# Performance work log

Hardware: AMD Instinct MI355X
Metric: run time of the kernel (lower is better)

## Reference

```python
import jax, jax.numpy as jnp
import numpy as np
import math

B, S, D = 4, 2048, 1024


def setup_inputs() -> dict:
    key = jax.random.key(0)
    k1, k2, k3 = jax.random.split(key, 3)
    X = jax.random.normal(k1, (B, S, D), dtype=jnp.float32)
    # causal mask, broadcast over batch (True = keep)
    mask = jnp.broadcast_to(jnp.tril(jnp.ones((S, S), dtype=bool)), (B, S, S))
    # torch nn.Linear weights: y = x @ W.T; init scale ~ 1/sqrt(D)
    WQK = jax.random.normal(k2, (D, D), dtype=jnp.float32) / math.sqrt(D)
    WOV = jax.random.normal(k3, (D, D), dtype=jnp.float32) / math.sqrt(D)
    return {"X": X, "mask": mask, "WQK": WQK, "WOV": WOV}


def reference(X, mask, WQK, WOV):
    d = X.shape[-1]
    Q = jnp.einsum('bsd,ed->bse', X, WQK)          # WQK(X) = X @ WQK.T
    Sc = jnp.einsum('bse,bte->bst', Q, X)          # shared-QK scores: Q @ X^T
    # NOTE: original multiplies by sqrt(d_model) (not divide) - faithful
    Sc = Sc * jnp.asarray(math.sqrt(d), Sc.dtype)
    Sc = jnp.where(mask, Sc, -jnp.inf)
    A = jax.nn.softmax(Sc, axis=-1)                # dropout p=0.0 -> identity
    V = jnp.einsum('bsd,ed->bse', X, WOV)          # WOV(X)
    Y = jnp.einsum('bst,bte->bse', A, V)
    return (X + Y, A)
```

## Files before the change

kernel.cpp:

```cpp
#include <hip/hip_runtime.h>
#include <hip/hip_fp16.h>
#include <math.h>

typedef _Float16 half_t;
typedef _Float16 h8_t __attribute__((ext_vector_type(8)));
typedef _Float16 h4_t __attribute__((ext_vector_type(4)));
typedef float f4_t __attribute__((ext_vector_type(4)));

#define MFMA16(a, b, c) __builtin_amdgcn_mfma_f32_16x16x32_f16(a, b, c, 0, 0, 0)

static constexpr int kB = 4;
static constexpr int kS = 2048;
static constexpr int kD = 1024;
static constexpr int BM = 128;
static constexpr int BN = 128;
static constexpr int BK = 32;
static constexpr int NT = 512;

__device__ __forceinline__ void gload16(const half_t* g, half_t* l) {
  __builtin_amdgcn_global_load_lds(
      (const __attribute__((address_space(1))) void*)g,
      (__attribute__((address_space(3))) void*)l, 16, 0, 0);
}

__device__ __forceinline__ void stage_tile(half_t* __restrict__ sm,
                                           const half_t* __restrict__ g, int ld) {
  const int t = threadIdx.x;
  const int r = t >> 2;
  const int c = ((t & 3) * 8) ^ ((((r >> 1) & 3)) << 3);
  gload16(&g[(size_t)r * ld + c], &sm[r * BK + (t & 3) * 8]);
}

template <bool SPLIT>
__device__ __forceinline__ void stage_all(half_t* buf, const half_t* Ahi,
                                          const half_t* Alo, int lda,
                                          const half_t* Bhi, const half_t* Blo,
                                          int ldb, size_t ko) {
  stage_tile(buf, Ahi + ko, lda);
  stage_tile(buf + BM * BK, Bhi + ko, ldb);
  if (SPLIT) {
    stage_tile(buf + 2 * BM * BK, Alo + ko, lda);
    stage_tile(buf + 3 * BM * BK, Blo + ko, ldb);
  }
}

template <bool SPLIT>
__device__ __forceinline__ void gemm_core(const half_t* __restrict__ Ahi,
                                          const half_t* __restrict__ Alo, int lda,
                                          const half_t* __restrict__ Bhi,
                                          const half_t* __restrict__ Blo, int ldb,
                                          int k_iters, half_t* sm, f4_t acc[4][2]) {
  constexpr int BUFSZ = (SPLIT ? 4 : 2) * BM * BK;
  const int lane = threadIdx.x & 63;
  const int wid = threadIdx.x >> 6;
  const int wm = (wid >> 2) * 64;
  const int wn = (wid & 3) * 32;
  const int fr = lane & 15;
  const int fk = (((lane >> 4) * 8) ^ (((lane >> 1) & 3) << 3));

  half_t* cur = sm;
  half_t* nxt = sm + BUFSZ;

  stage_all<SPLIT>(cur, Ahi, Alo, lda, Bhi, Blo, ldb, 0);
  asm volatile("s_waitcnt vmcnt(0)" ::: "memory");
  __builtin_amdgcn_s_barrier();

  for (int kk = 0; kk < k_iters; ++kk) {
    if (kk + 1 < k_iters)
      stage_all<SPLIT>(nxt, Ahi, Alo, lda, Bhi, Blo, ldb, (size_t)(kk + 1) * BK);
    const half_t* sAh = cur;
    const half_t* sBh = cur + BM * BK;
    const half_t* sAl = cur + 2 * BM * BK;
    const half_t* sBl = cur + 3 * BM * BK;
    h8_t a[4], b[2], al[4], bl[2];
#pragma unroll
    for (int i = 0; i < 4; ++i) {
      a[i] = *(const h8_t*)&sAh[(wm + i * 16 + fr) * BK + fk];
      if (SPLIT) al[i] = *(const h8_t*)&sAl[(wm + i * 16 + fr) * BK + fk];
    }
#pragma unroll
    for (int j = 0; j < 2; ++j) {
      b[j] = *(const h8_t*)&sBh[(wn + j * 16 + fr) * BK + fk];
      if (SPLIT) bl[j] = *(const h8_t*)&sBl[(wn + j * 16 + fr) * BK + fk];
    }
#pragma unroll
    for (int i = 0; i < 4; ++i)
#pragma unroll
      for (int j = 0; j < 2; ++j) {
        acc[i][j] = MFMA16(a[i], b[j], acc[i][j]);
        if (SPLIT) {
          acc[i][j] = MFMA16(a[i], bl[j], acc[i][j]);
          acc[i][j] = MFMA16(al[i], b[j], acc[i][j]);
        }
      }
    asm volatile("s_waitcnt vmcnt(0)" ::: "memory");
    __builtin_amdgcn_s_barrier();
    half_t* t = cur; cur = nxt; nxt = t;
  }
}

__global__ __launch_bounds__(NT) void gemm_q_kernel(
    const half_t* __restrict__ Xhi, const half_t* __restrict__ Xlo,
    const half_t* __restrict__ Whi, const half_t* __restrict__ Wlo,
    half_t* __restrict__ Qhi, half_t* __restrict__ Qlo) {
  __shared__ half_t sm[2 * 4 * BM * BK];
  const size_t arow = (size_t)blockIdx.y * BM;
  const size_t brow = (size_t)blockIdx.x * BN;
  f4_t acc[4][2] = {};
  gemm_core<true>(Xhi + arow * kD, Xlo + arow * kD, kD,
                  Whi + brow * kD, Wlo + brow * kD, kD, kD / BK, sm, acc);
  const int lane = threadIdx.x & 63;
  const int wid = threadIdx.x >> 6;
  const int wm = (wid >> 2) * 64, wn = (wid & 3) * 32;
  const int c16 = lane & 15, r4 = (lane >> 4) * 4;
#pragma unroll
  for (int i = 0; i < 4; ++i)
#pragma unroll
    for (int j = 0; j < 2; ++j)
#pragma unroll
      for (int r = 0; r < 4; ++r) {
        const size_t row = arow + wm + i * 16 + r4 + r;
        const size_t col = brow + wn + j * 16 + c16;
        const float q = acc[i][j][r];
        const half_t qh = (half_t)q;
        const half_t ql = (half_t)(q - (float)qh);
        const size_t idx = row * kD + col;
        Qhi[idx] = qh;
        Qlo[idx] = ql;
      }
}

__global__ __launch_bounds__(NT) void gemm_v_kernel(
    const half_t* __restrict__ Xhi, const half_t* __restrict__ Whi,
    half_t* __restrict__ Vt) {
  __shared__ half_t sm[2 * 2 * BM * BK];
  const size_t arow = (size_t)blockIdx.y * BM;
  const size_t brow = (size_t)blockIdx.x * BN;
  f4_t acc[4][2] = {};
  gemm_core<false>(Xhi + arow * kD, nullptr, kD, Whi + brow * kD, nullptr, kD,
                   kD / BK, sm, acc);
  const int lane = threadIdx.x & 63;
  const int wid = threadIdx.x >> 6;
  const int wm = (wid >> 2) * 64, wn = (wid & 3) * 32;
  const int c16 = lane & 15, r4 = (lane >> 4) * 4;
#pragma unroll
  for (int i = 0; i < 4; ++i)
#pragma unroll
    for (int j = 0; j < 2; ++j)
#pragma unroll
      for (int r = 0; r < 4; ++r) {
        const size_t row = arow + wm + i * 16 + r4 + r;
        const size_t col = brow + wn + j * 16 + c16;
        const size_t bi = row >> 11;
        const size_t s = row & 2047;
        Vt[bi * (size_t)kD * kS + col * kS + s] = (half_t)acc[i][j][r];
      }
}

__global__ __launch_bounds__(NT) void gemm_score_kernel(
    const half_t* __restrict__ Qhi, const half_t* __restrict__ Qlo,
    const half_t* __restrict__ Xhi, const half_t* __restrict__ Xlo,
    float* __restrict__ Sc) {
  const int tn = blockIdx.x, tm = blockIdx.y, bi = blockIdx.z;
  if (tn > tm) return;
  __shared__ half_t sm[2 * 4 * BM * BK];
  const size_t arow = (size_t)bi * kS + (size_t)tm * BM;
  const size_t brow = (size_t)bi * kS + (size_t)tn * BN;
  f4_t acc[4][2] = {};
  gemm_core<true>(Qhi + arow * kD, Qlo + arow * kD, kD,
                  Xhi + brow * kD, Xlo + brow * kD, kD, kD / BK, sm, acc);
  float* out = Sc + (size_t)bi * kS * kS;
  const int lane = threadIdx.x & 63;
  const int wid = threadIdx.x >> 6;
  const int wm = (wid >> 2) * 64, wn = (wid & 3) * 32;
  const int c16 = lane & 15, r4 = (lane >> 4) * 4;
#pragma unroll
  for (int i = 0; i < 4; ++i)
#pragma unroll
    for (int j = 0; j < 2; ++j)
#pragma unroll
      for (int r = 0; r < 4; ++r) {
        const int row = tm * BM + wm + i * 16 + r4 + r;
        const int col = tn * BN + wn + j * 16 + c16;
        out[(size_t)row * kS + col] = 32.0f * acc[i][j][r];
      }
}

__global__ __launch_bounds__(256) void softmax_kernel(float* __restrict__ A,
                                                      half_t* __restrict__ Ah) {
  const int rgl = blockIdx.x;
  const int s = rgl & 2047;
  float* row = A + (size_t)rgl * kS;
  half_t* hrow = Ah + (size_t)rgl * kS;
  const int tid = threadIdx.x;
  const int n = s + 1;
  float v[8];
  float mx = -INFINITY;
#pragma unroll
  for (int i = 0; i < 8; ++i) {
    const int t = tid + i * 256;
    v[i] = (t < n) ? row[t] : -INFINITY;
    mx = fmaxf(mx, v[i]);
  }
  for (int off = 32; off; off >>= 1) mx = fmaxf(mx, __shfl_xor(mx, off));
  __shared__ float red[8];
  const int lane = tid & 63, wid = tid >> 6;
  if (lane == 0) red[wid] = mx;
  __syncthreads();
  if (tid == 0) {
    float m = fmaxf(fmaxf(red[0], red[1]), fmaxf(red[2], red[3]));
    red[4] = m;
  }
  __syncthreads();
  mx = red[4];
  float sum = 0.0f;
#pragma unroll
  for (int i = 0; i < 8; ++i) {
    v[i] = (tid + i * 256 < n) ? __expf(v[i] - mx) : 0.0f;
    sum += v[i];
  }
  for (int off = 32; off; off >>= 1) sum += __shfl_xor(sum, off);
  __syncthreads();
  if (lane == 0) red[wid] = sum;
  __syncthreads();
  if (tid == 0) red[5] = 1.0f / (red[0] + red[1] + red[2] + red[3]);
  __syncthreads();
  const float inv = red[5];
#pragma unroll
  for (int i = 0; i < 8; ++i) {
    const int t = tid + i * 256;
    const float a = v[i] * inv;
    row[t] = a;
    hrow[t] = (half_t)a;
  }
}

__global__ __launch_bounds__(NT) void gemm_y_kernel(
    const half_t* __restrict__ Ah, const half_t* __restrict__ Vt,
    const float* __restrict__ X, float* __restrict__ Out) {
  __shared__ half_t sm[2 * 2 * BM * BK];
  const int tn = blockIdx.x, bi = blockIdx.z;
  const int tm = (kS / BM - 1) - blockIdx.y;
  const size_t abase = ((size_t)bi * kS + (size_t)tm * BM) * kS;
  const size_t bbase = ((size_t)bi * kD + (size_t)tn * BN) * kS;
  f4_t acc[4][2] = {};
  gemm_core<false>(Ah + abase, nullptr, kS, Vt + bbase, nullptr, kS,
                   (tm + 1) * BM / BK, sm, acc);
  const size_t obase = (size_t)bi * kS * kD;
  const int lane = threadIdx.x & 63;
  const int wid = threadIdx.x >> 6;
  const int wm = (wid >> 2) * 64, wn = (wid & 3) * 32;
  const int c16 = lane & 15, r4 = (lane >> 4) * 4;
#pragma unroll
  for (int i = 0; i < 4; ++i)
#pragma unroll
    for (int j = 0; j < 2; ++j)
#pragma unroll
      for (int r = 0; r < 4; ++r) {
        const size_t row = (size_t)tm * BM + wm + i * 16 + r4 + r;
        const size_t col = (size_t)tn * BN + wn + j * 16 + c16;
        const size_t idx = obase + row * kD + col;
        Out[idx] = X[idx] + acc[i][j][r];
      }
}

__global__ __launch_bounds__(256) void split_kernel(const float* __restrict__ x,
                                                    half_t* __restrict__ hi,
                                                    half_t* __restrict__ lo, int n4) {
  const int i = blockIdx.x * 256 + threadIdx.x;
  if (i >= n4) return;
  const float4 v = ((const float4*)x)[i];
  const float vv[4] = {v.x, v.y, v.z, v.w};
  h4_t h, l;
#pragma unroll
  for (int j = 0; j < 4; ++j) {
    const half_t hh = (half_t)vv[j];
    h[j] = hh;
    l[j] = (half_t)(vv[j] - (float)hh);
  }
  ((h4_t*)hi)[i] = h;
  ((h4_t*)lo)[i] = l;
}

__global__ __launch_bounds__(256) void cvt_kernel(const float* __restrict__ x,
                                                  half_t* __restrict__ hi, int n4) {
  const int i = blockIdx.x * 256 + threadIdx.x;
  if (i >= n4) return;
  const float4 v = ((const float4*)x)[i];
  h4_t h;
  h[0] = (half_t)v.x; h[1] = (half_t)v.y; h[2] = (half_t)v.z; h[3] = (half_t)v.w;
  ((h4_t*)hi)[i] = h;
}

extern "C" void kernel_launch(void* const* d_in, const int* in_sizes, int n_in,
                              void* d_out, int out_size, void* d_ws, size_t ws_size,
                              hipStream_t stream) {
  const float* X   = (const float*)d_in[0];
  const float* WQK = (const float*)d_in[2];
  const float* WOV = (const float*)d_in[3];

  constexpr size_t nX = (size_t)kB * kS * kD;
  constexpr size_t nW = (size_t)kD * kD;
  constexpr size_t nA = (size_t)kB * kS * kS;

  float* out0 = (float*)d_out;
  float* outA = out0 + nX;

  half_t* ws = (half_t*)d_ws;
  half_t* Xhi = ws; ws += nX;
  half_t* Xlo = ws; ws += nX;
  half_t* Qhi = ws; ws += nX;
  half_t* Qlo = ws; ws += nX;
  half_t* Whi = ws; ws += nW;
  half_t* Wlo = ws; ws += nW;
  half_t* WVh = ws; ws += nW;
  half_t* Vt  = ws; ws += nX;
  half_t* Ah  = ws; ws += nA;
  const size_t need_bytes = (size_t)((char*)ws - (char*)d_ws);
  if (ws_size < need_bytes) return;

  split_kernel<<<(int)(nX / 4 / 256), 256, 0, stream>>>(X, Xhi, Xlo, (int)(nX / 4));
  split_kernel<<<(int)(nW / 4 / 256), 256, 0, stream>>>(WQK, Whi, Wlo, (int)(nW / 4));
  cvt_kernel<<<(int)(nW / 4 / 256), 256, 0, stream>>>(WOV, WVh, (int)(nW / 4));

  gemm_q_kernel<<<dim3(kD / BN, kB * kS / BM), NT, 0, stream>>>(Xhi, Xlo, Whi, Wlo, Qhi, Qlo);
  gemm_v_kernel<<<dim3(kD / BN, kB * kS / BM), NT, 0, stream>>>(Xhi, WVh, Vt);
  gemm_score_kernel<<<dim3(kS / BN, kS / BM, kB), NT, 0, stream>>>(Qhi, Qlo, Xhi, Xlo, outA);
  softmax_kernel<<<kB * kS, 256, 0, stream>>>(outA, Ah);
  gemm_y_kernel<<<dim3(kD / BN, kS / BM, kB), NT, 0, stream>>>(Ah, Vt, X, out0);
}
```

Measured before the change: 380.0 us.

## Use 64x64 tiles for split-precision GEMMs, vectorize softmax, fuse prep kernels

The Q and score GEMMs, which use three-MFMA hi/lo split precision, move from 128x128 tiles with 512 threads to 64x64 tiles with 256 threads and a min-blocks launch bound, so more blocks run and the causal triangle is covered at finer granularity. The softmax now loads and stores contiguous 8-element chunks with vector accesses instead of strided scalar ones. The three input-conversion kernels are merged into one launch. Smaller tiles cut data reuse per block and raise global and LDS traffic per FLOP.

```diff
diff --git a/kernel.cpp b/kernel.cpp
--- a/kernel.cpp
+++ b/kernel.cpp
@@ -12,10 +12,7 @@
 static constexpr int kB = 4;
 static constexpr int kS = 2048;
 static constexpr int kD = 1024;
-static constexpr int BM = 128;
-static constexpr int BN = 128;
 static constexpr int BK = 32;
-static constexpr int NT = 512;
 
 __device__ __forceinline__ void gload16(const half_t* g, half_t* l) {
   __builtin_amdgcn_global_load_lds(
@@ -23,75 +20,68 @@
       (__attribute__((address_space(3))) void*)l, 16, 0, 0);
 }
 
-__device__ __forceinline__ void stage_tile(half_t* __restrict__ sm,
-                                           const half_t* __restrict__ g, int ld) {
+
+__device__ __forceinline__ void stage_tile64(half_t* __restrict__ sm,
+                                             const half_t* __restrict__ g, int ld) {
   const int t = threadIdx.x;
   const int r = t >> 2;
-  const int c = ((t & 3) * 8) ^ ((((r >> 1) & 3)) << 3);
-  gload16(&g[(size_t)r * ld + c], &sm[r * BK + (t & 3) * 8]);
-}
-
-template <bool SPLIT>
-__device__ __forceinline__ void stage_all(half_t* buf, const half_t* Ahi,
+  const int g8 = (t & 3) * 8;
+  const int c = g8 ^ (((r >> 1) & 3) << 3);
+  gload16(&g[(size_t)r * ld + c], &sm[r * BK + g8]);
+}
+
+__device__ __forceinline__ void stage4_64(half_t* buf, const half_t* Ahi,
                                           const half_t* Alo, int lda,
                                           const half_t* Bhi, const half_t* Blo,
                                           int ldb, size_t ko) {
-  stage_tile(buf, Ahi + ko, lda);
-  stage_tile(buf + BM * BK, Bhi + ko, ldb);
-  if (SPLIT) {
-    stage_tile(buf + 2 * BM * BK, Alo + ko, lda);
-    stage_tile(buf + 3 * BM * BK, Blo + ko, ldb);
-  }
-}
-
-template <bool SPLIT>
-__device__ __forceinline__ void gemm_core(const half_t* __restrict__ Ahi,
-                                          const half_t* __restrict__ Alo, int lda,
-                                          const half_t* __restrict__ Bhi,
-                                          const half_t* __restrict__ Blo, int ldb,
-                                          int k_iters, half_t* sm, f4_t acc[4][2]) {
-  constexpr int BUFSZ = (SPLIT ? 4 : 2) * BM * BK;
-  const int lane = threadIdx.x & 63;
-  const int wid = threadIdx.x >> 6;
-  const int wm = (wid >> 2) * 64;
-  const int wn = (wid & 3) * 32;
+  stage_tile64(buf,               Ahi + ko, lda);
+  stage_tile64(buf + 64 * BK,     Bhi + ko, ldb);
+  stage_tile64(buf + 2 * 64 * BK, Alo + ko, lda);
+  stage_tile64(buf + 3 * 64 * BK, Blo + ko, ldb);
+}
+
+__device__ __forceinline__ void gemm64_core(const half_t* __restrict__ Ahi,
+                                            const half_t* __restrict__ Alo, int lda,
+                                            const half_t* __restrict__ Bhi,
+                                            const half_t* __restrict__ Blo, int ldb,
+                                            int k_iters, half_t* sm, f4_t (&acc)[2][2]) {
+  constexpr int BUFSZ = 4 * 64 * BK;
+  const int lane = threadIdx.x & 63;
+  const int wid = threadIdx.x >> 6;
+  const int wm = (wid >> 1) * 32;
+  const int wn = (wid & 1) * 32;
   const int fr = lane & 15;
   const int fk = (((lane >> 4) * 8) ^ (((lane >> 1) & 3) << 3));
 
   half_t* cur = sm;
   half_t* nxt = sm + BUFSZ;
 
-  stage_all<SPLIT>(cur, Ahi, Alo, lda, Bhi, Blo, ldb, 0);
+  stage4_64(cur, Ahi, Alo, lda, Bhi, Blo, ldb, 0);
   asm volatile("s_waitcnt vmcnt(0)" ::: "memory");
   __builtin_amdgcn_s_barrier();
 
   for (int kk = 0; kk < k_iters; ++kk) {
     if (kk + 1 < k_iters)
-      stage_all<SPLIT>(nxt, Ahi, Alo, lda, Bhi, Blo, ldb, (size_t)(kk + 1) * BK);
+      stage4_64(nxt, Ahi, Alo, lda, Bhi, Blo, ldb, (size_t)(kk + 1) * BK);
     const half_t* sAh = cur;
-    const half_t* sBh = cur + BM * BK;
-    const half_t* sAl = cur + 2 * BM * BK;
-    const half_t* sBl = cur + 3 * BM * BK;
-    h8_t a[4], b[2], al[4], bl[2];
-#pragma unroll
-    for (int i = 0; i < 4; ++i) {
-      a[i] = *(const h8_t*)&sAh[(wm + i * 16 + fr) * BK + fk];
-      if (SPLIT) al[i] = *(const h8_t*)&sAl[(wm + i * 16 + fr) * BK + fk];
+    const half_t* sBh = cur + 64 * BK;
+    const half_t* sAl = cur + 2 * 64 * BK;
+    const half_t* sBl = cur + 3 * 64 * BK;
+    h8_t a[2], al[2], b[2], bl[2];
+#pragma unroll
+    for (int i = 0; i < 2; ++i) {
+      a[i]  = *(const h8_t*)&sAh[(wm + i * 16 + fr) * BK + fk];
+      al[i] = *(const h8_t*)&sAl[(wm + i * 16 + fr) * BK + fk];
+      b[i]  = *(const h8_t*)&sBh[(wn + i * 16 + fr) * BK + fk];
+      bl[i] = *(const h8_t*)&sBl[(wn + i * 16 + fr) * BK + fk];
     }
 #pragma unroll
-    for (int j = 0; j < 2; ++j) {
-      b[j] = *(const h8_t*)&sBh[(wn + j * 16 + fr) * BK + fk];
-      if (SPLIT) bl[j] = *(const h8_t*)&sBl[(wn + j * 16 + fr) * BK + fk];
-    }
-#pragma unroll
-    for (int i = 0; i < 4; ++i)
+    for (int i = 0; i < 2; ++i)
 #pragma unroll
       for (int j = 0; j < 2; ++j) {
         acc[i][j] = MFMA16(a[i], b[j], acc[i][j]);
-        if (SPLIT) {
-          acc[i][j] = MFMA16(a[i], bl[j], acc[i][j]);
-          acc[i][j] = MFMA16(al[i], b[j], acc[i][j]);
-        }
+        acc[i][j] = MFMA16(a[i], bl[j], acc[i][j]);
+        acc[i][j] = MFMA16(al[i], b[j], acc[i][j]);
       }
     asm volatile("s_waitcnt vmcnt(0)" ::: "memory");
     __builtin_amdgcn_s_barrier();
@@ -99,22 +89,22 @@
   }
 }
 
-__global__ __launch_bounds__(NT) void gemm_q_kernel(
+__global__ __launch_bounds__(256, 5) void gemm_q_kernel(
     const half_t* __restrict__ Xhi, const half_t* __restrict__ Xlo,
     const half_t* __restrict__ Whi, const half_t* __restrict__ Wlo,
     half_t* __restrict__ Qhi, half_t* __restrict__ Qlo) {
-  __shared__ half_t sm[2 * 4 * BM * BK];
-  const size_t arow = (size_t)blockIdx.y * BM;
-  const size_t brow = (size_t)blockIdx.x * BN;
-  f4_t acc[4][2] = {};
-  gemm_core<true>(Xhi + arow * kD, Xlo + arow * kD, kD,
-                  Whi + brow * kD, Wlo + brow * kD, kD, kD / BK, sm, acc);
-  const int lane = threadIdx.x & 63;
-  const int wid = threadIdx.x >> 6;
-  const int wm = (wid >> 2) * 64, wn = (wid & 3) * 32;
+  __shared__ half_t sm[2 * 4 * 64 * BK];
+  const size_t arow = (size_t)blockIdx.y * 64;
+  const size_t brow = (size_t)blockIdx.x * 64;
+  f4_t acc[2][2] = {};
+  gemm64_core(Xhi + arow * kD, Xlo + arow * kD, kD,
+              Whi + brow * kD, Wlo + brow * kD, kD, kD / BK, sm, acc);
+  const int lane = threadIdx.x & 63;
+  const int wid = threadIdx.x >> 6;
+  const int wm = (wid >> 1) * 32, wn = (wid & 1) * 32;
   const int c16 = lane & 15, r4 = (lane >> 4) * 4;
 #pragma unroll
-  for (int i = 0; i < 4; ++i)
+  for (int i = 0; i < 2; ++i)
 #pragma unroll
     for (int j = 0; j < 2; ++j)
 #pragma unroll
@@ -130,6 +120,95 @@
       }
 }
 
+__global__ __launch_bounds__(256, 5) void gemm_score_kernel(
+    const half_t* __restrict__ Qhi, const half_t* __restrict__ Qlo,
+    const half_t* __restrict__ Xhi, const half_t* __restrict__ Xlo,
+    float* __restrict__ Sc) {
+  const int tn = blockIdx.x, tm = blockIdx.y, bi = blockIdx.z;
+  if (tn > tm) return;
+  __shared__ half_t sm[2 * 4 * 64 * BK];
+  const size_t arow = (size_t)bi * kS + (size_t)tm * 64;
+  const size_t brow = (size_t)bi * kS + (size_t)tn * 64;
+  f4_t acc[2][2] = {};
+  gemm64_core(Qhi + arow * kD, Qlo + arow * kD, kD,
+              Xhi + brow * kD, Xlo + brow * kD, kD, kD / BK, sm, acc);
+  float* out = Sc + (size_t)bi * kS * kS;
+  const int lane = threadIdx.x & 63;
+  const int wid = threadIdx.x >> 6;
+  const int wm = (wid >> 1) * 32, wn = (wid & 1) * 32;
+  const int c16 = lane & 15, r4 = (lane >> 4) * 4;
+#pragma unroll
+  for (int i = 0; i < 2; ++i)
+#pragma unroll
+    for (int j = 0; j < 2; ++j)
+#pragma unroll
+      for (int r = 0; r < 4; ++r) {
+        const int row = tm * 64 + wm + i * 16 + r4 + r;
+        const int col = tn * 64 + wn + j * 16 + c16;
+        out[(size_t)row * kS + col] = 32.0f * acc[i][j][r];
+      }
+}
+
+static constexpr int BM = 128;
+static constexpr int BN = 128;
+static constexpr int NT = 512;
+
+__device__ __forceinline__ void stage_tile(half_t* __restrict__ sm,
+                                           const half_t* __restrict__ g, int ld) {
+  const int t = threadIdx.x;
+  const int r = t >> 2;
+  const int g8 = (t & 3) * 8;
+  const int c = g8 ^ (((r >> 1) & 3) << 3);
+  gload16(&g[(size_t)r * ld + c], &sm[r * BK + g8]);
+}
+
+__device__ __forceinline__ void stage_ab(half_t* buf, const half_t* A, int lda,
+                                         const half_t* B, int ldb, size_t ko) {
+  stage_tile(buf, A + ko, lda);
+  stage_tile(buf + BM * BK, B + ko, ldb);
+}
+
+__device__ __forceinline__ void gemm128_core(const half_t* __restrict__ A, int lda,
+                                             const half_t* __restrict__ B, int ldb,
+                                             int k_iters, half_t* sm, f4_t (&acc)[4][2]) {
+  constexpr int BUFSZ = 2 * BM * BK;
+  const int lane = threadIdx.x & 63;
+  const int wid = threadIdx.x >> 6;
+  const int wm = (wid >> 2) * 64;
+  const int wn = (wid & 3) * 32;
+  const int fr = lane & 15;
+  const int fk = (((lane >> 4) * 8) ^ (((lane >> 1) & 3) << 3));
+
+  half_t* cur = sm;
+  half_t* nxt = sm + BUFSZ;
+
+  stage_ab(cur, A, lda, B, ldb, 0);
+  asm volatile("s_waitcnt vmcnt(0)" ::: "memory");
+  __builtin_amdgcn_s_barrier();
+
+  for (int kk = 0; kk < k_iters; ++kk) {
+    if (kk + 1 < k_iters)
+      stage_ab(nxt, A, lda, B, ldb, (size_t)(kk + 1) * BK);
+    const half_t* sA = cur;
+    const half_t* sB = cur + BM * BK;
+    h8_t a[4], b[2];
+#pragma unroll
+    for (int i = 0; i < 4; ++i)
+      a[i] = *(const h8_t*)&sA[(wm + i * 16 + fr) * BK + fk];
+#pragma unroll
+    for (int j = 0; j < 2; ++j)
+      b[j] = *(const h8_t*)&sB[(wn + j * 16 + fr) * BK + fk];
+#pragma unroll
+    for (int i = 0; i < 4; ++i)
+#pragma unroll
+      for (int j = 0; j < 2; ++j)
+        acc[i][j] = MFMA16(a[i], b[j], acc[i][j]);
+    asm volatile("s_waitcnt vmcnt(0)" ::: "memory");
+    __builtin_amdgcn_s_barrier();
+    half_t* t = cur; cur = nxt; nxt = t;
+  }
+}
+
 __global__ __launch_bounds__(NT) void gemm_v_kernel(
     const half_t* __restrict__ Xhi, const half_t* __restrict__ Whi,
     half_t* __restrict__ Vt) {
@@ -137,8 +216,7 @@
   const size_t arow = (size_t)blockIdx.y * BM;
   const size_t brow = (size_t)blockIdx.x * BN;
   f4_t acc[4][2] = {};
-  gemm_core<false>(Xhi + arow * kD, nullptr, kD, Whi + brow * kD, nullptr, kD,
-                   kD / BK, sm, acc);
+  gemm128_core(Xhi + arow * kD, kD, Whi + brow * kD, kD, kD / BK, sm, acc);
   const int lane = threadIdx.x & 63;
   const int wid = threadIdx.x >> 6;
   const int wm = (wid >> 2) * 64, wn = (wid & 3) * 32;
@@ -155,84 +233,6 @@
         const size_t s = row & 2047;
         Vt[bi * (size_t)kD * kS + col * kS + s] = (half_t)acc[i][j][r];
       }
-}
-
-__global__ __launch_bounds__(NT) void gemm_score_kernel(
-    const half_t* __restrict__ Qhi, const half_t* __restrict__ Qlo,
-    const half_t* __restrict__ Xhi, const half_t* __restrict__ Xlo,
-    float* __restrict__ Sc) {
-  const int tn = blockIdx.x, tm = blockIdx.y, bi = blockIdx.z;
-  if (tn > tm) return;
-  __shared__ half_t sm[2 * 4 * BM * BK];
-  const size_t arow = (size_t)bi * kS + (size_t)tm * BM;
-  const size_t brow = (size_t)bi * kS + (size_t)tn * BN;
-  f4_t acc[4][2] = {};
-  gemm_core<true>(Qhi + arow * kD, Qlo + arow * kD, kD,
-                  Xhi + brow * kD, Xlo + brow * kD, kD, kD / BK, sm, acc);
-  float* out = Sc + (size_t)bi * kS * kS;
-  const int lane = threadIdx.x & 63;
-  const int wid = threadIdx.x >> 6;
-  const int wm = (wid >> 2) * 64, wn = (wid & 3) * 32;
-  const int c16 = lane & 15, r4 = (lane >> 4) * 4;
-#pragma unroll
-  for (int i = 0; i < 4; ++i)
-#pragma unroll
-    for (int j = 0; j < 2; ++j)
-#pragma unroll
-      for (int r = 0; r < 4; ++r) {
-        const int row = tm * BM + wm + i * 16 + r4 + r;
-        const int col = tn * BN + wn + j * 16 + c16;
-        out[(size_t)row * kS + col] = 32.0f * acc[i][j][r];
-      }
-}
-
-__global__ __launch_bounds__(256) void softmax_kernel(float* __restrict__ A,
-                                                      half_t* __restrict__ Ah) {
-  const int rgl = blockIdx.x;
-  const int s = rgl & 2047;
-  float* row = A + (size_t)rgl * kS;
-  half_t* hrow = Ah + (size_t)rgl * kS;
-  const int tid = threadIdx.x;
-  const int n = s + 1;
-  float v[8];
-  float mx = -INFINITY;
-#pragma unroll
-  for (int i = 0; i < 8; ++i) {
-    const int t = tid + i * 256;
-    v[i] = (t < n) ? row[t] : -INFINITY;
-    mx = fmaxf(mx, v[i]);
-  }
-  for (int off = 32; off; off >>= 1) mx = fmaxf(mx, __shfl_xor(mx, off));
-  __shared__ float red[8];
-  const int lane = tid & 63, wid = tid >> 6;
-  if (lane == 0) red[wid] = mx;
-  __syncthreads();
-  if (tid == 0) {
-    float m = fmaxf(fmaxf(red[0], red[1]), fmaxf(red[2], red[3]));
-    red[4] = m;
-  }
-  __syncthreads();
-  mx = red[4];
-  float sum = 0.0f;
-#pragma unroll
-  for (int i = 0; i < 8; ++i) {
-    v[i] = (tid + i * 256 < n) ? __expf(v[i] - mx) : 0.0f;
-    sum += v[i];
-  }
-  for (int off = 32; off; off >>= 1) sum += __shfl_xor(sum, off);
-  __syncthreads();
-  if (lane == 0) red[wid] = sum;
-  __syncthreads();
-  if (tid == 0) red[5] = 1.0f / (red[0] + red[1] + red[2] + red[3]);
-  __syncthreads();
-  const float inv = red[5];
-#pragma unroll
-  for (int i = 0; i < 8; ++i) {
-    const int t = tid + i * 256;
-    const float a = v[i] * inv;
-    row[t] = a;
-    hrow[t] = (half_t)a;
-  }
 }
 
 __global__ __launch_bounds__(NT) void gemm_y_kernel(
@@ -244,8 +244,7 @@
   const size_t abase = ((size_t)bi * kS + (size_t)tm * BM) * kS;
   const size_t bbase = ((size_t)bi * kD + (size_t)tn * BN) * kS;
   f4_t acc[4][2] = {};
-  gemm_core<false>(Ah + abase, nullptr, kS, Vt + bbase, nullptr, kS,
-                   (tm + 1) * BM / BK, sm, acc);
+  gemm128_core(Ah + abase, kS, Vt + bbase, kS, (tm + 1) * BM / BK, sm, acc);
   const size_t obase = (size_t)bi * kS * kD;
   const int lane = threadIdx.x & 63;
   const int wid = threadIdx.x >> 6;
@@ -264,32 +263,92 @@
       }
 }
 
-__global__ __launch_bounds__(256) void split_kernel(const float* __restrict__ x,
-                                                    half_t* __restrict__ hi,
-                                                    half_t* __restrict__ lo, int n4) {
+__global__ __launch_bounds__(256) void softmax_kernel(float* __restrict__ A,
+                                                      half_t* __restrict__ Ah) {
+  const int rgl = blockIdx.x;
+  const int s = rgl & 2047;
+  float* row = A + (size_t)rgl * kS;
+  half_t* hrow = Ah + (size_t)rgl * kS;
+  const int tid = threadIdx.x;
+  const int n = s + 1;
+  const int base = tid * 8;
+  f4_t v0 = ((const f4_t*)row)[tid * 2];
+  f4_t v1 = ((const f4_t*)row)[tid * 2 + 1];
+  float vv[8];
+#pragma unroll
+  for (int e = 0; e < 4; ++e) { vv[e] = v0[e]; vv[4 + e] = v1[e]; }
+  float mx = -INFINITY;
+#pragma unroll
+  for (int e = 0; e < 8; ++e) {
+    if (base + e >= n) vv[e] = -INFINITY;
+    mx = fmaxf(mx, vv[e]);
+  }
+  for (int off = 32; off; off >>= 1) mx = fmaxf(mx, __shfl_xor(mx, off));
+  __shared__ float red[8];
+  const int lane = tid & 63, wid = tid >> 6;
+  if (lane == 0) red[wid] = mx;
+  __syncthreads();
+  if (tid == 0) {
+    float m = fmaxf(fmaxf(red[0], red[1]), fmaxf(red[2], red[3]));
+    red[4] = m;
+  }
+  __syncthreads();
+  mx = red[4];
+  float sum = 0.0f;
+#pragma unroll
+  for (int e = 0; e < 8; ++e) {
+    vv[e] = (base + e < n) ? __expf(vv[e] - mx) : 0.0f;
+    sum += vv[e];
+  }
+  for (int off = 32; off; off >>= 1) sum += __shfl_xor(sum, off);
+  __syncthreads();
+  if (lane == 0) red[wid] = sum;
+  __syncthreads();
+  if (tid == 0) red[5] = 1.0f / (red[0] + red[1] + red[2] + red[3]);
+  __syncthreads();
+  const float inv = red[5];
+  f4_t o0, o1;
+  h8_t hv;
+#pragma unroll
+  for (int e = 0; e < 8; ++e) {
+    const float a = vv[e] * inv;
+    if (e < 4) o0[e] = a; else o1[e - 4] = a;
+    hv[e] = (half_t)a;
+  }
+  ((f4_t*)row)[tid * 2] = o0;
+  ((f4_t*)row)[tid * 2 + 1] = o1;
+  ((h8_t*)hrow)[tid] = hv;
+}
+
+__global__ __launch_bounds__(256) void prep_kernel(const float* __restrict__ X,
+                                                   const float* __restrict__ WQK,
+                                                   const float* __restrict__ WOV,
+                                                   half_t* __restrict__ Xhi,
+                                                   half_t* __restrict__ Xlo,
+                                                   half_t* __restrict__ Whi,
+                                                   half_t* __restrict__ Wlo,
+                                                   half_t* __restrict__ WVh) {
+  constexpr int nX4 = kB * kS * kD / 4;
+  constexpr int nW4 = kD * kD / 4;
   const int i = blockIdx.x * 256 + threadIdx.x;
-  if (i >= n4) return;
-  const float4 v = ((const float4*)x)[i];
-  const float vv[4] = {v.x, v.y, v.z, v.w};
+  const float* src;
+  half_t* hi;
+  half_t* lo;
+  int idx;
+  if (i < nX4) { src = X; hi = Xhi; lo = Xlo; idx = i; }
+  else if (i < nX4 + nW4) { src = WQK; hi = Whi; lo = Wlo; idx = i - nX4; }
+  else { src = WOV; hi = WVh; lo = nullptr; idx = i - nX4 - nW4; }
+  const float4 v = ((const float4*)src)[idx];
+  const float vvv[4] = {v.x, v.y, v.z, v.w};
   h4_t h, l;
 #pragma unroll
   for (int j = 0; j < 4; ++j) {
-    const half_t hh = (half_t)vv[j];
+    const half_t hh = (half_t)vvv[j];
     h[j] = hh;
-    l[j] = (half_t)(vv[j] - (float)hh);
-  }
-  ((h4_t*)hi)[i] = h;
-  ((h4_t*)lo)[i] = l;
-}
-
-__global__ __launch_bounds__(256) void cvt_kernel(const float* __restrict__ x,
-                                                  half_t* __restrict__ hi, int n4) {
-  const int i = blockIdx.x * 256 + threadIdx.x;
-  if (i >= n4) return;
-  const float4 v = ((const float4*)x)[i];
-  h4_t h;
-  h[0] = (half_t)v.x; h[1] = (half_t)v.y; h[2] = (half_t)v.z; h[3] = (half_t)v.w;
-  ((h4_t*)hi)[i] = h;
+    l[j] = (half_t)(vvv[j] - (float)hh);
+  }
+  ((h4_t*)hi)[idx] = h;
+  if (lo) ((h4_t*)lo)[idx] = l;
 }
 
 extern "C" void kernel_launch(void* const* d_in, const int* in_sizes, int n_in,
@@ -319,13 +378,12 @@
   const size_t need_bytes = (size_t)((char*)ws - (char*)d_ws);
   if (ws_size < need_bytes) return;
 
-  split_kernel<<<(int)(nX / 4 / 256), 256, 0, stream>>>(X, Xhi, Xlo, (int)(nX / 4));
-  split_kernel<<<(int)(nW / 4 / 256), 256, 0, stream>>>(WQK, Whi, Wlo, (int)(nW / 4));
-  cvt_kernel<<<(int)(nW / 4 / 256), 256, 0, stream>>>(WOV, WVh, (int)(nW / 4));
-
-  gemm_q_kernel<<<dim3(kD / BN, kB * kS / BM), NT, 0, stream>>>(Xhi, Xlo, Whi, Wlo, Qhi, Qlo);
+  constexpr int prep_items = (int)(nX / 4 + 2 * (nW / 4));
+  prep_kernel<<<prep_items / 256, 256, 0, stream>>>(X, WQK, WOV, Xhi, Xlo, Whi, Wlo, WVh);
+
+  gemm_q_kernel<<<dim3(kD / 64, kB * kS / 64), 256, 0, stream>>>(Xhi, Xlo, Whi, Wlo, Qhi, Qlo);
   gemm_v_kernel<<<dim3(kD / BN, kB * kS / BM), NT, 0, stream>>>(Xhi, WVh, Vt);
-  gemm_score_kernel<<<dim3(kS / BN, kS / BM, kB), NT, 0, stream>>>(Qhi, Qlo, Xhi, Xlo, outA);
+  gemm_score_kernel<<<dim3(kS / 64, kS / 64, kB), 256, 0, stream>>>(Qhi, Qlo, Xhi, Xlo, outA);
   softmax_kernel<<<kB * kS, 256, 0, stream>>>(outA, Ah);
   gemm_y_kernel<<<dim3(kD / BN, kS / BM, kB), NT, 0, stream>>>(Ah, Vt, X, out0);
 }
```

Measured after the change: 455.0 us. +19.7%, slower.

## Merge prep and Q/V GEMM launches, compact causal score grid, vectorize softmax

Applied to the files above, without the earlier changes.

Combines the three conversion kernels into one prep kernel and the Q and V projection GEMMs into one kernel, with an XCD-style block swizzle. The score GEMM now launches only the 544 lower-triangular tiles, decoding each tile index with a sqrt-based inverse, so no empty blocks are launched. Softmax switches to contiguous per-thread 8-element vector loads and stores. Together these cut launch count, idle blocks and uncoalesced scalar accesses, at the cost of divergent block roles and a float sqrt used for the tile decode.

```diff
diff --git a/kernel.cpp b/kernel.cpp
--- a/kernel.cpp
+++ b/kernel.cpp
@@ -27,8 +27,9 @@
                                            const half_t* __restrict__ g, int ld) {
   const int t = threadIdx.x;
   const int r = t >> 2;
-  const int c = ((t & 3) * 8) ^ ((((r >> 1) & 3)) << 3);
-  gload16(&g[(size_t)r * ld + c], &sm[r * BK + (t & 3) * 8]);
+  const int g8 = (t & 3) * 8;
+  const int c = g8 ^ (((r >> 1) & 3) << 3);
+  gload16(&g[(size_t)r * ld + c], &sm[r * BK + g8]);
 }
 
 template <bool SPLIT>
@@ -49,7 +50,7 @@
                                           const half_t* __restrict__ Alo, int lda,
                                           const half_t* __restrict__ Bhi,
                                           const half_t* __restrict__ Blo, int ldb,
-                                          int k_iters, half_t* sm, f4_t acc[4][2]) {
+                                          int k_iters, half_t* sm, f4_t (&acc)[4][2]) {
   constexpr int BUFSZ = (SPLIT ? 4 : 2) * BM * BK;
   const int lane = threadIdx.x & 63;
   const int wid = threadIdx.x >> 6;
@@ -99,70 +100,76 @@
   }
 }
 
-__global__ __launch_bounds__(NT) void gemm_q_kernel(
+__global__ __launch_bounds__(NT) void gemm_qv_kernel(
     const half_t* __restrict__ Xhi, const half_t* __restrict__ Xlo,
     const half_t* __restrict__ Whi, const half_t* __restrict__ Wlo,
-    half_t* __restrict__ Qhi, half_t* __restrict__ Qlo) {
+    const half_t* __restrict__ WVh,
+    half_t* __restrict__ Qhi, half_t* __restrict__ Qlo,
+    half_t* __restrict__ Vt) {
   __shared__ half_t sm[2 * 4 * BM * BK];
-  const size_t arow = (size_t)blockIdx.y * BM;
-  const size_t brow = (size_t)blockIdx.x * BN;
-  f4_t acc[4][2] = {};
-  gemm_core<true>(Xhi + arow * kD, Xlo + arow * kD, kD,
-                  Whi + brow * kD, Wlo + brow * kD, kD, kD / BK, sm, acc);
+  const int b = blockIdx.x;
+  const int swz = (b & 7) * 128 + (b >> 3);
+  const bool isq = swz < 512;
+  const int w = isq ? swz : swz - 512;
+  const size_t arow = (size_t)(w >> 3) * BM;
+  const size_t brow = (size_t)(w & 7) * BN;
+
   const int lane = threadIdx.x & 63;
   const int wid = threadIdx.x >> 6;
   const int wm = (wid >> 2) * 64, wn = (wid & 3) * 32;
   const int c16 = lane & 15, r4 = (lane >> 4) * 4;
-#pragma unroll
-  for (int i = 0; i < 4; ++i)
-#pragma unroll
-    for (int j = 0; j < 2; ++j)
-#pragma unroll
-      for (int r = 0; r < 4; ++r) {
-        const size_t row = arow + wm + i * 16 + r4 + r;
-        const size_t col = brow + wn + j * 16 + c16;
-        const float q = acc[i][j][r];
-        const half_t qh = (half_t)q;
-        const half_t ql = (half_t)(q - (float)qh);
-        const size_t idx = row * kD + col;
-        Qhi[idx] = qh;
-        Qlo[idx] = ql;
-      }
-}
-
-__global__ __launch_bounds__(NT) void gemm_v_kernel(
-    const half_t* __restrict__ Xhi, const half_t* __restrict__ Whi,
-    half_t* __restrict__ Vt) {
-  __shared__ half_t sm[2 * 2 * BM * BK];
-  const size_t arow = (size_t)blockIdx.y * BM;
-  const size_t brow = (size_t)blockIdx.x * BN;
-  f4_t acc[4][2] = {};
-  gemm_core<false>(Xhi + arow * kD, nullptr, kD, Whi + brow * kD, nullptr, kD,
-                   kD / BK, sm, acc);
-  const int lane = threadIdx.x & 63;
-  const int wid = threadIdx.x >> 6;
-  const int wm = (wid >> 2) * 64, wn = (wid & 3) * 32;
-  const int c16 = lane & 15, r4 = (lane >> 4) * 4;
-#pragma unroll
-  for (int i = 0; i < 4; ++i)
-#pragma unroll
-    for (int j = 0; j < 2; ++j)
-#pragma unroll
-      for (int r = 0; r < 4; ++r) {
-        const size_t row = arow + wm + i * 16 + r4 + r;
-        const size_t col = brow + wn + j * 16 + c16;
-        const size_t bi = row >> 11;
-        const size_t s = row & 2047;
-        Vt[bi * (size_t)kD * kS + col * kS + s] = (half_t)acc[i][j][r];
-      }
+
+  if (isq) {
+    f4_t acc[4][2] = {};
+    gemm_core<true>(Xhi + arow * kD, Xlo + arow * kD, kD,
+                    Whi + brow * kD, Wlo + brow * kD, kD, kD / BK, sm, acc);
+#pragma unroll
+    for (int i = 0; i < 4; ++i)
+#pragma unroll
+      for (int j = 0; j < 2; ++j)
+#pragma unroll
+        for (int r = 0; r < 4; ++r) {
+          const size_t row = arow + wm + i * 16 + r4 + r;
+          const size_t col = brow + wn + j * 16 + c16;
+          const float q = acc[i][j][r];
+          const half_t qh = (half_t)q;
+          const half_t ql = (half_t)(q - (float)qh);
+          const size_t idx = row * kD + col;
+          Qhi[idx] = qh;
+          Qlo[idx] = ql;
+        }
+  } else {
+    f4_t acc[4][2] = {};
+    gemm_core<false>(Xhi + arow * kD, nullptr, kD,
+                     WVh + brow * kD, nullptr, kD, kD / BK, sm, acc);
+#pragma unroll
+    for (int i = 0; i < 4; ++i)
+#pragma unroll
+      for (int j = 0; j < 2; ++j)
+#pragma unroll
+        for (int r = 0; r < 4; ++r) {
+          const size_t row = arow + wm + i * 16 + r4 + r;
+          const size_t col = brow + wn + j * 16 + c16;
+          const size_t bi = row >> 11;
+          const size_t s = row & 2047;
+          Vt[bi * (size_t)kD * kS + col * kS + s] = (half_t)acc[i][j][r];
+        }
+  }
 }
 
 __global__ __launch_bounds__(NT) void gemm_score_kernel(
     const half_t* __restrict__ Qhi, const half_t* __restrict__ Qlo,
     const half_t* __restrict__ Xhi, const half_t* __restrict__ Xlo,
     float* __restrict__ Sc) {
-  const int tn = blockIdx.x, tm = blockIdx.y, bi = blockIdx.z;
-  if (tn > tm) return;
+  const int b = blockIdx.x;
+  const int swz = (b & 7) * 68 + (b >> 3);
+  const int bi = swz / 136;
+  const int t = swz - bi * 136;
+  int tm = (int)((sqrtf(8.0f * (float)t + 1.0f) - 1.0f) * 0.5f);
+  if ((tm + 1) * (tm + 2) / 2 <= t) ++tm;
+  if (tm * (tm + 1) / 2 > t) --tm;
+  const int tn = t - tm * (tm + 1) / 2;
+
   __shared__ half_t sm[2 * 4 * BM * BK];
   const size_t arow = (size_t)bi * kS + (size_t)tm * BM;
   const size_t brow = (size_t)bi * kS + (size_t)tn * BN;
@@ -194,13 +201,17 @@
   half_t* hrow = Ah + (size_t)rgl * kS;
   const int tid = threadIdx.x;
   const int n = s + 1;
-  float v[8];
+  const int base = tid * 8;
+  f4_t v0 = ((const f4_t*)row)[tid * 2];
+  f4_t v1 = ((const f4_t*)row)[tid * 2 + 1];
+  float vv[8];
+#pragma unroll
+  for (int e = 0; e < 4; ++e) { vv[e] = v0[e]; vv[4 + e] = v1[e]; }
   float mx = -INFINITY;
 #pragma unroll
-  for (int i = 0; i < 8; ++i) {
-    const int t = tid + i * 256;
-    v[i] = (t < n) ? row[t] : -INFINITY;
-    mx = fmaxf(mx, v[i]);
+  for (int e = 0; e < 8; ++e) {
+    if (base + e >= n) vv[e] = -INFINITY;
+    mx = fmaxf(mx, vv[e]);
   }
   for (int off = 32; off; off >>= 1) mx = fmaxf(mx, __shfl_xor(mx, off));
   __shared__ float red[8];
@@ -215,9 +226,9 @@
   mx = red[4];
   float sum = 0.0f;
 #pragma unroll
-  for (int i = 0; i < 8; ++i) {
-    v[i] = (tid + i * 256 < n) ? __expf(v[i] - mx) : 0.0f;
-    sum += v[i];
+  for (int e = 0; e < 8; ++e) {
+    vv[e] = (base + e < n) ? __expf(vv[e] - mx) : 0.0f;
+    sum += vv[e];
   }
   for (int off = 32; off; off >>= 1) sum += __shfl_xor(sum, off);
   __syncthreads();
@@ -226,13 +237,17 @@
   if (tid == 0) red[5] = 1.0f / (red[0] + red[1] + red[2] + red[3]);
   __syncthreads();
   const float inv = red[5];
-#pragma unroll
-  for (int i = 0; i < 8; ++i) {
-    const int t = tid + i * 256;
-    const float a = v[i] * inv;
-    row[t] = a;
-    hrow[t] = (half_t)a;
-  }
+  f4_t o0, o1;
+  h8_t hv;
+#pragma unroll
+  for (int e = 0; e < 8; ++e) {
+    const float a = vv[e] * inv;
+    if (e < 4) o0[e] = a; else o1[e - 4] = a;
+    hv[e] = (half_t)a;
+  }
+  ((f4_t*)row)[tid * 2] = o0;
+  ((f4_t*)row)[tid * 2 + 1] = o1;
+  ((h8_t*)hrow)[tid] = hv;
 }
 
 __global__ __launch_bounds__(NT) void gemm_y_kernel(
@@ -264,32 +279,35 @@
       }
 }
 
-__global__ __launch_bounds__(256) void split_kernel(const float* __restrict__ x,
-                                                    half_t* __restrict__ hi,
-                                                    half_t* __restrict__ lo, int n4) {
+__global__ __launch_bounds__(256) void prep_kernel(const float* __restrict__ X,
+                                                   const float* __restrict__ WQK,
+                                                   const float* __restrict__ WOV,
+                                                   half_t* __restrict__ Xhi,
+                                                   half_t* __restrict__ Xlo,
+                                                   half_t* __restrict__ Whi,
+                                                   half_t* __restrict__ Wlo,
+                                                   half_t* __restrict__ WVh) {
+  constexpr int nX4 = kB * kS * kD / 4;
+  constexpr int nW4 = kD * kD / 4;
   const int i = blockIdx.x * 256 + threadIdx.x;
-  if (i >= n4) return;
-  const float4 v = ((const float4*)x)[i];
-  const float vv[4] = {v.x, v.y, v.z, v.w};
+  const float* src;
+  half_t* hi;
+  half_t* lo;
+  int idx;
+  if (i < nX4) { src = X; hi = Xhi; lo = Xlo; idx = i; }
+  else if (i < nX4 + nW4) { src = WQK; hi = Whi; lo = Wlo; idx = i - nX4; }
+  else { src = WOV; hi = WVh; lo = nullptr; idx = i - nX4 - nW4; }
+  const float4 v = ((const float4*)src)[idx];
+  const float vvv[4] = {v.x, v.y, v.z, v.w};
   h4_t h, l;
 #pragma unroll
   for (int j = 0; j < 4; ++j) {
-    const half_t hh = (half_t)vv[j];
+    const half_t hh = (half_t)vvv[j];
     h[j] = hh;
-    l[j] = (half_t)(vv[j] - (float)hh);
-  }
-  ((h4_t*)hi)[i] = h;
-  ((h4_t*)lo)[i] = l;
-}
-
-__global__ __launch_bounds__(256) void cvt_kernel(const float* __restrict__ x,
-                                                  half_t* __restrict__ hi, int n4) {
-  const int i = blockIdx.x * 256 + threadIdx.x;
-  if (i >= n4) return;
-  const float4 v = ((const float4*)x)[i];
-  h4_t h;
-  h[0] = (half_t)v.x; h[1] = (half_t)v.y; h[2] = (half_t)v.z; h[3] = (half_t)v.w;
-  ((h4_t*)hi)[i] = h;
+    l[j] = (half_t)(vvv[j] - (float)hh);
+  }
+  ((h4_t*)hi)[idx] = h;
+  if (lo) ((h4_t*)lo)[idx] = l;
 }
 
 extern "C" void kernel_launch(void* const* d_in, const int* in_sizes, int n_in,
@@ -319,13 +337,11 @@
   const size_t need_bytes = (size_t)((char*)ws - (char*)d_ws);
   if (ws_size < need_bytes) return;
 
-  split_kernel<<<(int)(nX / 4 / 256), 256, 0, stream>>>(X, Xhi, Xlo, (int)(nX / 4));
-  split_kernel<<<(int)(nW / 4 / 256), 256, 0, stream>>>(WQK, Whi, Wlo, (int)(nW / 4));
-  cvt_kernel<<<(int)(nW / 4 / 256), 256, 0, stream>>>(WOV, WVh, (int)(nW / 4));
-
-  gemm_q_kernel<<<dim3(kD / BN, kB * kS / BM), NT, 0, stream>>>(Xhi, Xlo, Whi, Wlo, Qhi, Qlo);
-  gemm_v_kernel<<<dim3(kD / BN, kB * kS / BM), NT, 0, stream>>>(Xhi, WVh, Vt);
-  gemm_score_kernel<<<dim3(kS / BN, kS / BM, kB), NT, 0, stream>>>(Qhi, Qlo, Xhi, Xlo, outA);
+  constexpr int prep_items = (int)(nX / 4 + 2 * (nW / 4));
+  prep_kernel<<<prep_items / 256, 256, 0, stream>>>(X, WQK, WOV, Xhi, Xlo, Whi, Wlo, WVh);
+
+  gemm_qv_kernel<<<1024, NT, 0, stream>>>(Xhi, Xlo, Whi, Wlo, WVh, Qhi, Qlo, Vt);
+  gemm_score_kernel<<<544, NT, 0, stream>>>(Qhi, Qlo, Xhi, Xlo, outA);
   softmax_kernel<<<kB * kS, 256, 0, stream>>>(outA, Ah);
   gemm_y_kernel<<<dim3(kD / BN, kS / BM, kB), NT, 0, stream>>>(Ah, Vt, X, out0);
 }
```

Result: slower. 389.8 us (+2.6%).
